# Kernel tuning notes

Hardware: AMD Instinct MI355X
Metric: run time of the kernel (lower is better)

The kernel has to match this reference:

```python
import jax, jax.numpy as jnp
import numpy as np
import math

N_NODES = 50000
N_EDGES = 800000
F_IN = 32
HID = 64


def _layernorm(x, g, b, eps=1e-5):
    mu = x.mean(-1, keepdims=True)
    var = ((x - mu) ** 2).mean(-1, keepdims=True)
    return (x - mu) / jnp.sqrt(var + eps) * g + b


def _tconv(x, src, dst, Wq, bq, Wk, bk, Wv, bv, Ws, heads):
    # PyG TransformerConv (concat=True, root_weight=True, bias=False on skip)
    N = x.shape[0]
    C = Wq.shape[1] // heads
    q = (x @ Wq + bq).reshape(N, heads, C)[dst]  # [E,H,C] gathered at targets
    k = (x @ Wk + bk).reshape(N, heads, C)[src]  # [E,H,C] gathered at sources
    v = (x @ Wv + bv).reshape(N, heads, C)[src]
    scores = (q * k).sum(-1) / math.sqrt(C)      # [E,H]
    m = jax.ops.segment_max(scores, dst, num_segments=N)   # [N,H]
    p = jnp.exp(scores - m[dst])
    denom = jax.ops.segment_sum(p, dst, num_segments=N)
    alpha = p / (denom[dst] + 1e-16)             # segment softmax over in-edges
    agg = jax.ops.segment_sum(v * alpha[..., None], dst, num_segments=N)
    return agg.reshape(N, heads * C) + x @ Ws    # + skip (no bias)


def setup_inputs() -> dict:
    key = jax.random.key(0)
    ks = iter(jax.random.split(key, 64))
    def rn(shape, s=0.1):
        return jax.random.normal(next(ks), shape, jnp.float32) * s
    inp = {
        "x": rn((N_NODES, F_IN), 1.0),
        "edge_index": jax.random.randint(next(ks), (2, N_EDGES), 0, N_NODES, dtype=jnp.int32),
        "ln0_g": jnp.ones((F_IN,), jnp.float32),
        "ln0_b": jnp.zeros((F_IN,), jnp.float32),
    }
    dims = [F_IN, HID, HID]
    for l in range(3):
        d = dims[l]
        inp[f"Wq{l}"] = rn((d, HID)); inp[f"bq{l}"] = rn((HID,), 0.05)
        inp[f"Wk{l}"] = rn((d, HID)); inp[f"bk{l}"] = rn((HID,), 0.05)
        inp[f"Wv{l}"] = rn((d, HID)); inp[f"bv{l}"] = rn((HID,), 0.05)
        inp[f"Ws{l}"] = rn((d, HID))
        inp[f"g{l}"] = jnp.ones((HID,), jnp.float32)
        inp[f"b{l}"] = jnp.zeros((HID,), jnp.float32)
    inp["Wr1"] = rn((HID, HID // 2)); inp["br1"] = jnp.zeros((HID // 2,), jnp.float32)
    inp["Wr2"] = rn((HID // 2, 1));   inp["br2"] = jnp.zeros((1,), jnp.float32)
    inp["Wt1"] = rn((HID, HID // 2)); inp["bt1"] = jnp.zeros((HID // 2,), jnp.float32)
    inp["Wt2"] = rn((HID // 2, 1));   inp["bt2"] = jnp.zeros((1,), jnp.float32)
    return inp


def reference(x, edge_index, ln0_g, ln0_b,
              Wq0, bq0, Wk0, bk0, Wv0, bv0, Ws0, g0, b0,
              Wq1, bq1, Wk1, bk1, Wv1, bv1, Ws1, g1, b1,
              Wq2, bq2, Wk2, bk2, Wv2, bv2, Ws2, g2, b2,
              Wr1, br1, Wr2, br2, Wt1, bt1, Wt2, bt2):
    src, dst = edge_index[0], edge_index[1]
    h = _layernorm(x, ln0_g, ln0_b)
    layers = [
        (Wq0, bq0, Wk0, bk0, Wv0, bv0, Ws0, g0, b0, 4),
        (Wq1, bq1, Wk1, bk1, Wv1, bv1, Ws1, g1, b1, 4),
        (Wq2, bq2, Wk2, bk2, Wv2, bv2, Ws2, g2, b2, 1),
    ]
    for i, (Wq, bq, Wk, bk, Wv, bv, Ws, g, b, heads) in enumerate(layers):
        x_res = h if h.shape[-1] == HID else None
        h = _tconv(h, src, dst, Wq, bq, Wk, bk, Wv, bv, Ws, heads)
        h = _layernorm(h, g, b)
        if x_res is not None and i > 0:
            h = h + 0.1 * x_res
        if i < len(layers) - 1:
            h = jax.nn.relu(h)  # dropout is identity in eval mode
    rtt = jax.nn.relu(h @ Wr1 + br1) @ Wr2 + br2      # [N,1]
    retrans = jax.nn.relu(h @ Wt1 + bt1) @ Wt2 + bt2  # [N,1]
    return jnp.concatenate([rtt, retrans], axis=1)    # [N,2]
```

## Files before the change

kernel.cpp:

```cpp
#include <hip/hip_runtime.h>
#include <hip/hip_bf16.h>
#include <hip/hip_fp16.h>
#include <math.h>

#define N_NODES 50000
#define N_EDGES 800000
#define HID 64
#define NBK 196
#define EPB 1024
#define SB  ((N_EDGES + EPB - 1) / EPB)
#define FLAT (NBK * SB)
#define SCAN_B ((FLAT + 255) / 256)

#define QKVS0_BLKS 3125

#define LN0_BLKS   6250
#define HIST_BLKS  SB
#define WP0_BLKS   32
#define WP12_BLKS  64
#define PREP_BLKS  (LN0_BLKS + HIST_BLKS + WP0_BLKS + 2 * WP12_BLKS)

typedef __attribute__((ext_vector_type(8))) short short8;
typedef __attribute__((ext_vector_type(4))) float float4v;
typedef __attribute__((ext_vector_type(2))) float float2v;

__device__ __forceinline__ unsigned short f32_to_bf16_rne(float f) {
    unsigned int u = __float_as_uint(f);
    unsigned int r = u + 0x7fffu + ((u >> 16) & 1u);
    return (unsigned short)(r >> 16);
}

__device__ __forceinline__ unsigned int f32_to_fp8_byte(float f) {
    return (unsigned int)__builtin_amdgcn_cvt_pk_fp8_f32(f, f, 0, false) & 0xffu;
}
template <bool HI>
__device__ __forceinline__ float2v fp8x2_to_f32(unsigned int w) {
    return __builtin_amdgcn_cvt_pk_f32_fp8((int)w, HI);
}
__device__ __forceinline__ float2 h2_to_f32(unsigned int w) {
    __half2 h = *reinterpret_cast<__half2*>(&w);
    return __half22float2(h);
}

__device__ __forceinline__ void ln0_body(int b, int t,
        const float* __restrict__ x, const float* __restrict__ g,
        const float* __restrict__ bb, float* __restrict__ h0) {
    int lane = t & 63;
    int n = b * 8 + (t >> 6) * 2 + (lane >> 5);
    int c = lane & 31;
    float v = x[n * 32 + c];
    float s = v;
    #pragma unroll
    for (int off = 1; off < 32; off <<= 1) s += __shfl_xor(s, off);
    float mu = s * (1.0f / 32.0f);
    float d = v - mu;
    float vs = d * d;
    #pragma unroll
    for (int off = 1; off < 32; off <<= 1) vs += __shfl_xor(vs, off);
    float var = vs * (1.0f / 32.0f);
    h0[n * 32 + c] = d * rsqrtf(var + 1e-5f) * g[c] + bb[c];
}

__device__ __forceinline__ void wprep_body(int idx, int KS,
        const float* __restrict__ Wq, const float* __restrict__ Wk,
        const float* __restrict__ Wv, const float* __restrict__ Ws,
        unsigned short* __restrict__ Wp) {
    int j = idx & 7;
    int lane = (idx >> 3) & 63;
    int ts = idx >> 9;
    int s = ts % KS;
    int tile = ts / KS;
    int which = tile >> 2;
    int slice = tile & 3;
    int k = s * 32 + ((lane >> 4) * 8) + j;
    int col = slice * 16 + (lane & 15);
    const float* W = (which == 0) ? Wq : (which == 1) ? Wk : (which == 2) ? Wv : Ws;
    Wp[idx] = f32_to_bf16_rne(W[k * 64 + col]);
}

__global__ __launch_bounds__(256) void prep_kernel(
        const float* __restrict__ x, const float* __restrict__ ln0g,
        const float* __restrict__ ln0b, float* __restrict__ h0,
        const int* __restrict__ dst, int* __restrict__ ghist,
        const float* __restrict__ Wq0, const float* __restrict__ Wk0,
        const float* __restrict__ Wv0, const float* __restrict__ Ws0,
        unsigned short* __restrict__ Wp0,
        const float* __restrict__ Wq1, const float* __restrict__ Wk1,
        const float* __restrict__ Wv1, const float* __restrict__ Ws1,
        unsigned short* __restrict__ Wp1,
        const float* __restrict__ Wq2, const float* __restrict__ Wk2,
        const float* __restrict__ Wv2, const float* __restrict__ Ws2,
        unsigned short* __restrict__ Wp2) {
    __shared__ int hist[NBK];
    int b = blockIdx.x;
    int t = threadIdx.x;
    if (b < LN0_BLKS) {
        ln0_body(b, t, x, ln0g, ln0b, h0);
    } else if (b < LN0_BLKS + HIST_BLKS) {
        int i = b - LN0_BLKS;
        for (int k = t; k < NBK; k += 256) hist[k] = 0;
        __syncthreads();
        int e0 = i * EPB;
        #pragma unroll
        for (int r = 0; r < EPB / 256; r++) {
            int e = e0 + r * 256 + t;
            if (e < N_EDGES) atomicAdd(&hist[dst[e] >> 8], 1);
        }
        __syncthreads();
        for (int k = t; k < NBK; k += 256) ghist[k * SB + i] = hist[k];
    } else if (b < LN0_BLKS + HIST_BLKS + WP0_BLKS) {
        int idx = (b - LN0_BLKS - HIST_BLKS) * 256 + t;
        wprep_body(idx, 1, Wq0, Wk0, Wv0, Ws0, Wp0);
    } else if (b < LN0_BLKS + HIST_BLKS + WP0_BLKS + WP12_BLKS) {
        int idx = (b - LN0_BLKS - HIST_BLKS - WP0_BLKS) * 256 + t;
        wprep_body(idx, 2, Wq1, Wk1, Wv1, Ws1, Wp1);
    } else {
        int idx = (b - LN0_BLKS - HIST_BLKS - WP0_BLKS - WP12_BLKS) * 256 + t;
        wprep_body(idx, 2, Wq2, Wk2, Wv2, Ws2, Wp2);
    }
}

__global__ void scan1_kernel(const int* __restrict__ ghist, int* __restrict__ csum) {
    int f = blockIdx.x * 256 + threadIdx.x;
    int v = (f < FLAT) ? ghist[f] : 0;
    #pragma unroll
    for (int off = 1; off < 64; off <<= 1) v += __shfl_xor(v, off);
    __shared__ int ws[4];
    if ((threadIdx.x & 63) == 0) ws[threadIdx.x >> 6] = v;
    __syncthreads();
    if (threadIdx.x == 0) csum[blockIdx.x] = ws[0] + ws[1] + ws[2] + ws[3];
}

__global__ void scan2_kernel(const int* __restrict__ csum, int* __restrict__ coff,
                             int* __restrict__ bbase, int* __restrict__ row_ptr) {
    int lane = threadIdx.x;
    int carry = 0;
    for (int base = 0; base < SCAN_B; base += 64) {
        int i = base + lane;
        int v = (i < SCAN_B) ? csum[i] : 0;
        int incl = v;
        #pragma unroll
        for (int off = 1; off < 64; off <<= 1) {
            int tt = __shfl_up(incl, off);
            if (lane >= off) incl += tt;
        }
        if (i < SCAN_B) coff[i] = carry + incl - v;
        carry += __shfl(incl, 63);
    }
    if (lane == 0) { bbase[NBK] = N_EDGES; row_ptr[N_NODES] = N_EDGES; }
}

__global__ void scan3_kernel(const int* __restrict__ ghist, const int* __restrict__ coff,
                             int* __restrict__ goff, int* __restrict__ bbase) {
    int f = blockIdx.x * 256 + threadIdx.x;
    int lane = threadIdx.x & 63;
    int w = threadIdx.x >> 6;
    int v = (f < FLAT) ? ghist[f] : 0;
    int incl = v;
    #pragma unroll
    for (int off = 1; off < 64; off <<= 1) {
        int tt = __shfl_up(incl, off);
        if (lane >= off) incl += tt;
    }
    __shared__ int ws[4];
    if (lane == 63) ws[w] = incl;
    __syncthreads();
    int woff = 0;
    #pragma unroll
    for (int k = 0; k < 4; k++) if (k < w) woff += ws[k];
    int excl = coff[blockIdx.x] + woff + incl - v;
    if (f < FLAT) {
        goff[f] = excl;
        if (f % SB == 0) bbase[f / SB] = excl;
    }
}

template <int D>
__device__ __forceinline__ void qkvs_body(int bid, int t,
        const float* __restrict__ h,
        const unsigned short* __restrict__ Wp,
        const float* __restrict__ bq, const float* __restrict__ bk,
        const float* __restrict__ bv, float scale,
        float* __restrict__ Qf, float* __restrict__ Sf,
        unsigned int* __restrict__ K8, uint2* __restrict__ Vh) {
    constexpr int KS = D / 32;
    int lane = t & 63;
    int w = t >> 6;
    int n0 = bid * 16;
    int n16 = lane & 15;
    int quad = lane >> 4;
    int col = w * 16 + n16;

    short8 afrag[KS];
    #pragma unroll
    for (int s = 0; s < KS; s++) {
        const float* hp = &h[(n0 + n16) * D + s * 32 + quad * 8];
        float4 a0 = *(const float4*)hp;
        float4 a1 = *(const float4*)(hp + 4);
        short8 af;
        af[0] = (short)f32_to_bf16_rne(a0.x);
        af[1] = (short)f32_to_bf16_rne(a0.y);
        af[2] = (short)f32_to_bf16_rne(a0.z);
        af[3] = (short)f32_to_bf16_rne(a0.w);
        af[4] = (short)f32_to_bf16_rne(a1.x);
        af[5] = (short)f32_to_bf16_rne(a1.y);
        af[6] = (short)f32_to_bf16_rne(a1.z);
        af[7] = (short)f32_to_bf16_rne(a1.w);
        afrag[s] = af;
    }

    float4v accs[4];
    #pragma unroll
    for (int which = 0; which < 4; which++) {
        float4v acc = {0.0f, 0.0f, 0.0f, 0.0f};
        int tile = which * 4 + w;
        #pragma unroll
        for (int s = 0; s < KS; s++) {
            short8 bfrag = *(const short8*)&Wp[((tile * KS + s) * 64 + lane) * 8];
            acc = __builtin_amdgcn_mfma_f32_16x16x32_bf16(afrag[s], bfrag, acc, 0, 0, 0);
        }
        accs[which] = acc;
    }

    float bqc = bq[col], bkc = bk[col], bvc = bv[col];
    int j = n16 & 3;
    int mword = (col >> 2);

    #pragma unroll
    for (int r = 0; r < 4; r++) {
        int node = n0 + quad * 4 + r;
        Qf[node * 64 + col] = (accs[0][r] + bqc) * scale;
        Sf[node * 64 + col] = accs[3][r];
        unsigned int ku = f32_to_fp8_byte(accs[1][r] + bkc) << (8 * j);
        ku |= __shfl_xor(ku, 1); ku |= __shfl_xor(ku, 2);
        unsigned int hb = (unsigned int)__half_as_ushort(__float2half_rn(accs[2][r] + bvc));
        unsigned int vx = (j < 2) ? (hb << (16 * j)) : 0u;
        unsigned int vy = (j >= 2) ? (hb << (16 * (j - 2))) : 0u;
        vx |= __shfl_xor(vx, 1); vx |= __shfl_xor(vx, 2);
        vy |= __shfl_xor(vy, 1); vy |= __shfl_xor(vy, 2);
        if (j == 0) {
            K8[node * 16 + mword] = ku;
            Vh[node * 16 + mword] = make_uint2(vx, vy);
        }
    }
}

template <int D>
__global__ __launch_bounds__(256) void qkvs_mfma_kernel(
        const float* __restrict__ h,
        const unsigned short* __restrict__ Wp,
        const float* __restrict__ bq, const float* __restrict__ bk,
        const float* __restrict__ bv, float scale,
        float* __restrict__ Qf, float* __restrict__ Sf,
        unsigned int* __restrict__ K8, uint2* __restrict__ Vh) {
    qkvs_body<D>(blockIdx.x, threadIdx.x, h, Wp, bq, bk, bv, scale, Qf, Sf, K8, Vh);
}

__global__ __launch_bounds__(256) void scatter_qkvs0_kernel(
        const int* __restrict__ src, const int* __restrict__ dst,
        const int* __restrict__ goff, int2* __restrict__ ebkt,
        const float* __restrict__ h, const unsigned short* __restrict__ Wp,
        const float* __restrict__ bq, const float* __restrict__ bk,
        const float* __restrict__ bv, float scale,
        float* __restrict__ Qf, float* __restrict__ Sf,
        unsigned int* __restrict__ K8, uint2* __restrict__ Vh) {
    __shared__ int hist[NBK];
    int t = threadIdx.x;
    if (blockIdx.x < SB) {
        int i = blockIdx.x;
        for (int k = t; k < NBK; k += 256) hist[k] = 0;
        __syncthreads();
        int e0 = i * EPB;
        #pragma unroll
        for (int r = 0; r < EPB / 256; r++) {
            int e = e0 + r * 256 + t;
            if (e < N_EDGES) {
                int s = src[e], d = dst[e];
                int k = d >> 8;
                int rank = atomicAdd(&hist[k], 1);
                ebkt[goff[k * SB + i] + rank] = make_int2(s, d);
            }
        }
    } else {
        qkvs_body<32>(blockIdx.x - SB, t, h, Wp, bq, bk, bv, scale, Qf, Sf, K8, Vh);
    }
}

__global__ __launch_bounds__(256) void bucket_build_kernel(
        const int2* __restrict__ ebkt, const int* __restrict__ bbase,
        int* __restrict__ row_ptr, int* __restrict__ colb) {
    __shared__ int ldeg[256];
    __shared__ int lcur[256];
    __shared__ int wsum[4];
    int b = blockIdx.x;
    int t = threadIdx.x;
    int cbase = bbase[b];
    int cnt = bbase[b + 1] - cbase;

    ldeg[t] = 0;
    __syncthreads();
    for (int i = t; i < cnt; i += 256) {
        int2 e = ebkt[cbase + i];
        atomicAdd(&ldeg[e.y & 255], 1);
    }
    __syncthreads();

    int lane = t & 63;
    int w = t >> 6;
    int v = ldeg[t];
    int incl = v;
    #pragma unroll
    for (int off = 1; off < 64; off <<= 1) {
        int tt = __shfl_up(incl, off);
        if (lane >= off) incl += tt;
    }
    if (lane == 63) wsum[w] = incl;
    __syncthreads();
    int woff = 0;
    #pragma unroll
    for (int k = 0; k < 4; k++) if (k < w) woff += wsum[k];
    int excl = woff + incl - v;

    int node = b * 256 + t;
    if (node < N_NODES) row_ptr[node] = cbase + excl;
    lcur[t] = excl;
    __syncthreads();

    for (int i = t; i < cnt; i += 256) {
        int2 e = ebkt[cbase + i];
        int r = atomicAdd(&lcur[e.y & 255], 1);
        colb[cbase + r] = e.x;
    }
}

template <int HEADS, bool RES, bool RELU, bool HEAD>
__global__ __launch_bounds__(256) void agg_kernel(
                           const float* __restrict__ Qf,
                           const float* __restrict__ Sf,
                           const unsigned int* __restrict__ K8,
                           const uint2* __restrict__ Vh,
                           const int* __restrict__ row_ptr, const int* __restrict__ colb,
                           const float* __restrict__ g, const float* __restrict__ b,
                           const float* __restrict__ h_in, float* __restrict__ h_out,
                           const float* __restrict__ Wr1, const float* __restrict__ br1,
                           const float* __restrict__ Wr2, const float* __restrict__ br2,
                           const float* __restrict__ Wt1, const float* __restrict__ bt1,
                           const float* __restrict__ Wt2, const float* __restrict__ bt2,
                           float* __restrict__ out) {
    constexpr int C = HID / HEADS;
    int lane = threadIdx.x & 63;
    int m = lane & 15;
    int grp = lane >> 4;
    int n = blockIdx.x * 4 + (threadIdx.x >> 6);

    float4 q4 = *(const float4*)&Qf[n * 64 + 4 * m];

    int beg = row_ptr[n], end = row_ptr[n + 1];

    float ssum = 0.0f;
    float acc0 = 0.0f, acc1 = 0.0f, acc2 = 0.0f, acc3 = 0.0f;

    for (int base = beg; base < end; base += 64) {
        int limit = min(end - base, 64);
        int src_l = (base + lane < end) ? colb[base + lane] : 0;
        for (int sub = 0; sub < limit; sub += 16) {
            int e0 = sub + grp, e1 = sub + 4 + grp, e2 = sub + 8 + grp, e3 = sub + 12 + grp;
            int s0 = __shfl(src_l, e0);
            int s1 = __shfl(src_l, e1);
            int s2 = __shfl(src_l, e2);
            int s3 = __shfl(src_l, e3);
            bool v0ok = e0 < limit, v1ok = e1 < limit, v2ok = e2 < limit, v3ok = e3 < limit;
            unsigned int ka0 = 0, ka1 = 0, ka2 = 0, ka3 = 0;
            uint2 va0 = make_uint2(0, 0), va1 = va0, va2 = va0, va3 = va0;
            if (v0ok) { ka0 = K8[(size_t)s0 * 16 + m]; va0 = Vh[(size_t)s0 * 16 + m]; }
            if (v1ok) { ka1 = K8[(size_t)s1 * 16 + m]; va1 = Vh[(size_t)s1 * 16 + m]; }
            if (v2ok) { ka2 = K8[(size_t)s2 * 16 + m]; va2 = Vh[(size_t)s2 * 16 + m]; }
            if (v3ok) { ka3 = K8[(size_t)s3 * 16 + m]; va3 = Vh[(size_t)s3 * 16 + m]; }

            float2v k0a = fp8x2_to_f32<false>(ka0), k0b = fp8x2_to_f32<true>(ka0);
            float2v k1a = fp8x2_to_f32<false>(ka1), k1b = fp8x2_to_f32<true>(ka1);
            float2v k2a = fp8x2_to_f32<false>(ka2), k2b = fp8x2_to_f32<true>(ka2);
            float2v k3a = fp8x2_to_f32<false>(ka3), k3b = fp8x2_to_f32<true>(ka3);

            float t0 = fmaf(q4.x, k0a.x, fmaf(q4.y, k0a.y,
                       fmaf(q4.z, k0b.x, q4.w * k0b.y)));
            float t1 = fmaf(q4.x, k1a.x, fmaf(q4.y, k1a.y,
                       fmaf(q4.z, k1b.x, q4.w * k1b.y)));
            float t2 = fmaf(q4.x, k2a.x, fmaf(q4.y, k2a.y,
                       fmaf(q4.z, k2b.x, q4.w * k2b.y)));
            float t3 = fmaf(q4.x, k3a.x, fmaf(q4.y, k3a.y,
                       fmaf(q4.z, k3b.x, q4.w * k3b.y)));
            #pragma unroll
            for (int off = 1; off < C / 4; off <<= 1) {
                t0 += __shfl_xor(t0, off);
                t1 += __shfl_xor(t1, off);
                t2 += __shfl_xor(t2, off);
                t3 += __shfl_xor(t3, off);
            }
            float p0 = v0ok ? __expf(t0) : 0.0f;
            float p1 = v1ok ? __expf(t1) : 0.0f;
            float p2 = v2ok ? __expf(t2) : 0.0f;
            float p3 = v3ok ? __expf(t3) : 0.0f;
            ssum += (p0 + p1) + (p2 + p3);

            float2 v0a = h2_to_f32(va0.x), v0b = h2_to_f32(va0.y);
            float2 v1a = h2_to_f32(va1.x), v1b = h2_to_f32(va1.y);
            float2 v2a = h2_to_f32(va2.x), v2b = h2_to_f32(va2.y);
            float2 v3a = h2_to_f32(va3.x), v3b = h2_to_f32(va3.y);

            acc0 = fmaf(p0, v0a.x, fmaf(p1, v1a.x,
                   fmaf(p2, v2a.x, fmaf(p3, v3a.x, acc0))));
            acc1 = fmaf(p0, v0a.y, fmaf(p1, v1a.y,
                   fmaf(p2, v2a.y, fmaf(p3, v3a.y, acc1))));
            acc2 = fmaf(p0, v0b.x, fmaf(p1, v1b.x,
                   fmaf(p2, v2b.x, fmaf(p3, v3b.x, acc2))));
            acc3 = fmaf(p0, v0b.y, fmaf(p1, v1b.y,
                   fmaf(p2, v2b.y, fmaf(p3, v3b.y, acc3))));
        }
    }

    #pragma unroll
    for (int off = 16; off < 64; off <<= 1) {
        ssum += __shfl_xor(ssum, off);
        acc0 += __shfl_xor(acc0, off);
        acc1 += __shfl_xor(acc1, off);
        acc2 += __shfl_xor(acc2, off);
        acc3 += __shfl_xor(acc3, off);
    }

    float inv = 1.0f / (ssum + 1e-16f);
    float4 sv = *(const float4*)&Sf[n * 64 + 4 * m];
    float o0 = fmaf(acc0, inv, sv.x);
    float o1 = fmaf(acc1, inv, sv.y);
    float o2 = fmaf(acc2, inv, sv.z);
    float o3 = fmaf(acc3, inv, sv.w);

    float s = (o0 + o1) + (o2 + o3);
    #pragma unroll
    for (int off = 1; off < 16; off <<= 1) s += __shfl_xor(s, off);
    float mu = s * (1.0f / 64.0f);
    float d0 = o0 - mu, d1 = o1 - mu, d2 = o2 - mu, d3 = o3 - mu;
    float vs = (d0 * d0 + d1 * d1) + (d2 * d2 + d3 * d3);
    #pragma unroll
    for (int off = 1; off < 16; off <<= 1) vs += __shfl_xor(vs, off);
    float rstd = rsqrtf(vs * (1.0f / 64.0f) + 1e-5f);

    float4 gv = *(const float4*)&g[4 * m];
    float4 bv = *(const float4*)&b[4 * m];
    float y0 = d0 * rstd * gv.x + bv.x;
    float y1 = d1 * rstd * gv.y + bv.y;
    float y2 = d2 * rstd * gv.z + bv.z;
    float y3 = d3 * rstd * gv.w + bv.w;
    if (RES) {
        float4 rv = *(const float4*)&h_in[n * 64 + 4 * m];
        y0 = fmaf(0.1f, rv.x, y0);
        y1 = fmaf(0.1f, rv.y, y1);
        y2 = fmaf(0.1f, rv.z, y2);
        y3 = fmaf(0.1f, rv.w, y3);
    }
    if (RELU) {
        y0 = fmaxf(y0, 0.0f); y1 = fmaxf(y1, 0.0f);
        y2 = fmaxf(y2, 0.0f); y3 = fmaxf(y3, 0.0f);
    }

    if (!HEAD) {
        if (grp == 0) {
            float4 yv = make_float4(y0, y1, y2, y3);
            *(float4*)&h_out[n * 64 + 4 * m] = yv;
        }
    } else {
        __shared__ float sh[4][HID];
        int wave = threadIdx.x >> 6;
        if (grp == 0) {
            float4 yv = make_float4(y0, y1, y2, y3);
            *(float4*)&sh[wave][4 * m] = yv;
        }
        __syncthreads();
        int half = lane >> 5;
        int j = lane & 31;
        const float* W1 = half ? Wt1 : Wr1;
        const float* b1 = half ? bt1 : br1;
        const float* W2 = half ? Wt2 : Wr2;
        const float* b2v = half ? bt2 : br2;
        float a = b1[j];
        #pragma unroll 8
        for (int i = 0; i < 64; i++) a = fmaf(sh[wave][i], W1[i * 32 + j], a);
        a = fmaxf(a, 0.0f);
        float r = a * W2[j];
        #pragma unroll
        for (int off = 1; off < 32; off <<= 1) r += __shfl_xor(r, off);
        if (j == 0) out[n * 2 + half] = r + b2v[0];
    }
}

extern "C" void kernel_launch(void* const* d_in, const int* in_sizes, int n_in,
                              void* d_out, int out_size, void* d_ws, size_t ws_size,
                              hipStream_t stream) {
    const float* x    = (const float*)d_in[0];
    const int*   ei   = (const int*)d_in[1];
    const int*   src  = ei;
    const int*   dst  = ei + N_EDGES;
    const float* ln0g = (const float*)d_in[2];
    const float* ln0b = (const float*)d_in[3];

    const float* P[27];
    for (int i = 0; i < 27; i++) P[i] = (const float*)d_in[4 + i];
    const float* Wr1 = (const float*)d_in[31];
    const float* br1 = (const float*)d_in[32];
    const float* Wr2 = (const float*)d_in[33];
    const float* br2 = (const float*)d_in[34];
    const float* Wt1 = (const float*)d_in[35];
    const float* bt1 = (const float*)d_in[36];
    const float* Wt2 = (const float*)d_in[37];
    const float* bt2 = (const float*)d_in[38];

    float* out = (float*)d_out;

    float* hbuf0 = (float*)d_ws;
    float* hbuf1 = hbuf0 + N_NODES * 64;
    float* Qf    = hbuf1 + N_NODES * 64;
    float* Sf    = Qf + N_NODES * 64;
    unsigned int* K8 = (unsigned int*)(Sf + N_NODES * 64);
    uint2* Vh    = (uint2*)(K8 + N_NODES * 16);
    int* row_ptr = (int*)(Vh + N_NODES * 16);
    int* colb    = row_ptr + (N_NODES + 1);
    int* ghist   = colb + N_EDGES;
    int* goff    = ghist + FLAT;
    int* csum    = goff + FLAT;
    int* coff    = csum + SCAN_B;
    int* bbase   = coff + SCAN_B;
    unsigned short* Wp0 = (unsigned short*)(bbase + NBK + 1);
    unsigned short* Wp1 = Wp0 + 16 * 1 * 512;
    unsigned short* Wp2 = Wp1 + 16 * 2 * 512;
    int2* ebkt = (int2*)hbuf1;

    prep_kernel<<<PREP_BLKS, 256, 0, stream>>>(x, ln0g, ln0b, hbuf0,
        dst, ghist,
        P[0],  P[2],  P[4],  P[6],  Wp0,
        P[9],  P[11], P[13], P[15], Wp1,
        P[18], P[20], P[22], P[24], Wp2);
    scan1_kernel<<<SCAN_B, 256, 0, stream>>>(ghist, csum);
    scan2_kernel<<<1, 64, 0, stream>>>(csum, coff, bbase, row_ptr);
    scan3_kernel<<<SCAN_B, 256, 0, stream>>>(ghist, coff, goff, bbase);
    scatter_qkvs0_kernel<<<SB + QKVS0_BLKS, 256, 0, stream>>>(src, dst, goff, ebkt,
        hbuf0, Wp0, P[1], P[3], P[5], 0.25f, Qf, Sf, K8, Vh);
    bucket_build_kernel<<<NBK, 256, 0, stream>>>(ebkt, bbase, row_ptr, colb);

    agg_kernel<4, false, true, false><<<12500, 256, 0, stream>>>(Qf, Sf, K8, Vh,
        row_ptr, colb, P[7], P[8], nullptr, hbuf1,
        Wr1, br1, Wr2, br2, Wt1, bt1, Wt2, bt2, out);

    qkvs_mfma_kernel<64><<<3125, 256, 0, stream>>>(hbuf1, Wp1,
        P[10], P[12], P[14], 0.25f, Qf, Sf, K8, Vh);
    agg_kernel<4, true, true, false><<<12500, 256, 0, stream>>>(Qf, Sf, K8, Vh,
        row_ptr, colb, P[16], P[17], hbuf1, hbuf0,
        Wr1, br1, Wr2, br2, Wt1, bt1, Wt2, bt2, out);

    qkvs_mfma_kernel<64><<<3125, 256, 0, stream>>>(hbuf0, Wp2,
        P[19], P[21], P[23], 0.125f, Qf, Sf, K8, Vh);
    agg_kernel<1, true, false, true><<<12500, 256, 0, stream>>>(Qf, Sf, K8, Vh,
        row_ptr, colb, P[25], P[26], hbuf0, hbuf1,
        Wr1, br1, Wr2, br2, Wt1, bt1, Wt2, bt2, out);
}
```

Before: 330.1 us.

## Split edge scoring into separate per-edge kernel and pack Q/skip as bf16

Moves the attention score computation (q·k dot and exp) out of the node-centric aggregation into a new edge-parallel score kernel that writes per-edge exp scores to a buffer. Q and the skip projection are stored packed as bf16 pairs in one word array instead of two fp32 arrays, and the CSR column array now stores (src,dst) pairs so the score kernel knows each edge's target. The aggregation then only gathers V and the precomputed scores. This trades an extra kernel launch per layer and a large intermediate score buffer write/read for better load balance and fewer shuffles in the aggregation, and lowers Q/skip precision to bf16.

```diff
diff --git a/kernel.cpp b/kernel.cpp
--- a/kernel.cpp
+++ b/kernel.cpp
@@ -13,6 +13,7 @@
 #define SCAN_B ((FLAT + 255) / 256)
 
 #define QKVS0_BLKS 3125
+#define SCORE_BLKS ((N_EDGES * 4) / 256)
 
 #define LN0_BLKS   6250
 #define HIST_BLKS  SB
@@ -181,7 +182,7 @@
         const unsigned short* __restrict__ Wp,
         const float* __restrict__ bq, const float* __restrict__ bk,
         const float* __restrict__ bv, float scale,
-        float* __restrict__ Qf, float* __restrict__ Sf,
+        unsigned int* __restrict__ QS,
         unsigned int* __restrict__ K8, uint2* __restrict__ Vh) {
     constexpr int KS = D / 32;
     int lane = t & 63;
@@ -229,8 +230,9 @@
     #pragma unroll
     for (int r = 0; r < 4; r++) {
         int node = n0 + quad * 4 + r;
-        Qf[node * 64 + col] = (accs[0][r] + bqc) * scale;
-        Sf[node * 64 + col] = accs[3][r];
+        unsigned int qw = f32_to_bf16_rne((accs[0][r] + bqc) * scale);
+        unsigned int sw = f32_to_bf16_rne(accs[3][r]);
+        QS[node * 64 + col] = (sw << 16) | qw;
         unsigned int ku = f32_to_fp8_byte(accs[1][r] + bkc) << (8 * j);
         ku |= __shfl_xor(ku, 1); ku |= __shfl_xor(ku, 2);
         unsigned int hb = (unsigned int)__half_as_ushort(__float2half_rn(accs[2][r] + bvc));
@@ -251,9 +253,9 @@
         const unsigned short* __restrict__ Wp,
         const float* __restrict__ bq, const float* __restrict__ bk,
         const float* __restrict__ bv, float scale,
-        float* __restrict__ Qf, float* __restrict__ Sf,
+        unsigned int* __restrict__ QS,
         unsigned int* __restrict__ K8, uint2* __restrict__ Vh) {
-    qkvs_body<D>(blockIdx.x, threadIdx.x, h, Wp, bq, bk, bv, scale, Qf, Sf, K8, Vh);
+    qkvs_body<D>(blockIdx.x, threadIdx.x, h, Wp, bq, bk, bv, scale, QS, K8, Vh);
 }
 
 __global__ __launch_bounds__(256) void scatter_qkvs0_kernel(
@@ -262,7 +264,7 @@
         const float* __restrict__ h, const unsigned short* __restrict__ Wp,
         const float* __restrict__ bq, const float* __restrict__ bk,
         const float* __restrict__ bv, float scale,
-        float* __restrict__ Qf, float* __restrict__ Sf,
+        unsigned int* __restrict__ QS,
         unsigned int* __restrict__ K8, uint2* __restrict__ Vh) {
     __shared__ int hist[NBK];
     int t = threadIdx.x;
@@ -282,13 +284,13 @@
             }
         }
     } else {
-        qkvs_body<32>(blockIdx.x - SB, t, h, Wp, bq, bk, bv, scale, Qf, Sf, K8, Vh);
+        qkvs_body<32>(blockIdx.x - SB, t, h, Wp, bq, bk, bv, scale, QS, K8, Vh);
     }
 }
 
 __global__ __launch_bounds__(256) void bucket_build_kernel(
         const int2* __restrict__ ebkt, const int* __restrict__ bbase,
-        int* __restrict__ row_ptr, int* __restrict__ colb) {
+        int* __restrict__ row_ptr, int2* __restrict__ colb2) {
     __shared__ int ldeg[256];
     __shared__ int lcur[256];
     __shared__ int wsum[4];
@@ -329,17 +331,69 @@
     for (int i = t; i < cnt; i += 256) {
         int2 e = ebkt[cbase + i];
         int r = atomicAdd(&lcur[e.y & 255], 1);
-        colb[cbase + r] = e.x;
+        colb2[cbase + r] = e;
+    }
+}
+
+template <int HEADS>
+__global__ __launch_bounds__(256) void score_kernel(
+        const unsigned int* __restrict__ QS,
+        const unsigned int* __restrict__ K8,
+        const int2* __restrict__ colb2,
+        float* __restrict__ p) {
+    int gid = blockIdx.x * 256 + threadIdx.x;
+    int e = gid >> 2;
+    int slot = gid & 3;
+    int2 ed = colb2[e];
+    const unsigned int* qp = &QS[(size_t)ed.y * 64 + slot * 16];
+    uint4 qa = *(const uint4*)qp;
+    uint4 qb = *(const uint4*)(qp + 4);
+    uint4 qc = *(const uint4*)(qp + 8);
+    uint4 qd = *(const uint4*)(qp + 12);
+    uint4 kw = *(const uint4*)&K8[(size_t)ed.x * 16 + slot * 4];
+
+    float2v k0 = fp8x2_to_f32<false>(kw.x), k1 = fp8x2_to_f32<true>(kw.x);
+    float2v k2 = fp8x2_to_f32<false>(kw.y), k3 = fp8x2_to_f32<true>(kw.y);
+    float2v k4 = fp8x2_to_f32<false>(kw.z), k5 = fp8x2_to_f32<true>(kw.z);
+    float2v k6 = fp8x2_to_f32<false>(kw.w), k7 = fp8x2_to_f32<true>(kw.w);
+
+    float t;
+    t =      __uint_as_float(qa.x << 16) * k0.x;
+    t = fmaf(__uint_as_float(qa.y << 16), k0.y, t);
+    t = fmaf(__uint_as_float(qa.z << 16), k1.x, t);
+    t = fmaf(__uint_as_float(qa.w << 16), k1.y, t);
+    t = fmaf(__uint_as_float(qb.x << 16), k2.x, t);
+    t = fmaf(__uint_as_float(qb.y << 16), k2.y, t);
+    t = fmaf(__uint_as_float(qb.z << 16), k3.x, t);
+    t = fmaf(__uint_as_float(qb.w << 16), k3.y, t);
+    t = fmaf(__uint_as_float(qc.x << 16), k4.x, t);
+    t = fmaf(__uint_as_float(qc.y << 16), k4.y, t);
+    t = fmaf(__uint_as_float(qc.z << 16), k5.x, t);
+    t = fmaf(__uint_as_float(qc.w << 16), k5.y, t);
+    t = fmaf(__uint_as_float(qd.x << 16), k6.x, t);
+    t = fmaf(__uint_as_float(qd.y << 16), k6.y, t);
+    t = fmaf(__uint_as_float(qd.z << 16), k7.x, t);
+    t = fmaf(__uint_as_float(qd.w << 16), k7.y, t);
+
+    if (HEADS == 1) {
+        t += __shfl_xor(t, 1);
+        t += __shfl_xor(t, 2);
+    }
+    float pv = __expf(t);
+    if (HEADS == 4) {
+        p[(size_t)e * 4 + slot] = pv;
+    } else {
+        if (slot == 0) p[e] = pv;
     }
 }
 
 template <int HEADS, bool RES, bool RELU, bool HEAD>
 __global__ __launch_bounds__(256) void agg_kernel(
-                           const float* __restrict__ Qf,
-                           const float* __restrict__ Sf,
-                           const unsigned int* __restrict__ K8,
+                           const unsigned int* __restrict__ QS,
                            const uint2* __restrict__ Vh,
-                           const int* __restrict__ row_ptr, const int* __restrict__ colb,
+                           const float* __restrict__ p,
+                           const int2* __restrict__ colb2,
+                           const int* __restrict__ row_ptr,
                            const float* __restrict__ g, const float* __restrict__ b,
                            const float* __restrict__ h_in, float* __restrict__ h_out,
                            const float* __restrict__ Wr1, const float* __restrict__ br1,
@@ -347,75 +401,35 @@
                            const float* __restrict__ Wt1, const float* __restrict__ bt1,
                            const float* __restrict__ Wt2, const float* __restrict__ bt2,
                            float* __restrict__ out) {
-    constexpr int C = HID / HEADS;
     int lane = threadIdx.x & 63;
     int m = lane & 15;
     int grp = lane >> 4;
     int n = blockIdx.x * 4 + (threadIdx.x >> 6);
-
-    float4 q4 = *(const float4*)&Qf[n * 64 + 4 * m];
+    int hsel = m >> 2;
 
     int beg = row_ptr[n], end = row_ptr[n + 1];
 
     float ssum = 0.0f;
     float acc0 = 0.0f, acc1 = 0.0f, acc2 = 0.0f, acc3 = 0.0f;
 
-    for (int base = beg; base < end; base += 64) {
-        int limit = min(end - base, 64);
-        int src_l = (base + lane < end) ? colb[base + lane] : 0;
-        for (int sub = 0; sub < limit; sub += 16) {
-            int e0 = sub + grp, e1 = sub + 4 + grp, e2 = sub + 8 + grp, e3 = sub + 12 + grp;
-            int s0 = __shfl(src_l, e0);
-            int s1 = __shfl(src_l, e1);
-            int s2 = __shfl(src_l, e2);
-            int s3 = __shfl(src_l, e3);
-            bool v0ok = e0 < limit, v1ok = e1 < limit, v2ok = e2 < limit, v3ok = e3 < limit;
-            unsigned int ka0 = 0, ka1 = 0, ka2 = 0, ka3 = 0;
-            uint2 va0 = make_uint2(0, 0), va1 = va0, va2 = va0, va3 = va0;
-            if (v0ok) { ka0 = K8[(size_t)s0 * 16 + m]; va0 = Vh[(size_t)s0 * 16 + m]; }
-            if (v1ok) { ka1 = K8[(size_t)s1 * 16 + m]; va1 = Vh[(size_t)s1 * 16 + m]; }
-            if (v2ok) { ka2 = K8[(size_t)s2 * 16 + m]; va2 = Vh[(size_t)s2 * 16 + m]; }
-            if (v3ok) { ka3 = K8[(size_t)s3 * 16 + m]; va3 = Vh[(size_t)s3 * 16 + m]; }
-
-            float2v k0a = fp8x2_to_f32<false>(ka0), k0b = fp8x2_to_f32<true>(ka0);
-            float2v k1a = fp8x2_to_f32<false>(ka1), k1b = fp8x2_to_f32<true>(ka1);
-            float2v k2a = fp8x2_to_f32<false>(ka2), k2b = fp8x2_to_f32<true>(ka2);
-            float2v k3a = fp8x2_to_f32<false>(ka3), k3b = fp8x2_to_f32<true>(ka3);
-
-            float t0 = fmaf(q4.x, k0a.x, fmaf(q4.y, k0a.y,
-                       fmaf(q4.z, k0b.x, q4.w * k0b.y)));
-            float t1 = fmaf(q4.x, k1a.x, fmaf(q4.y, k1a.y,
-                       fmaf(q4.z, k1b.x, q4.w * k1b.y)));
-            float t2 = fmaf(q4.x, k2a.x, fmaf(q4.y, k2a.y,
-                       fmaf(q4.z, k2b.x, q4.w * k2b.y)));
-            float t3 = fmaf(q4.x, k3a.x, fmaf(q4.y, k3a.y,
-                       fmaf(q4.z, k3b.x, q4.w * k3b.y)));
-            #pragma unroll
-            for (int off = 1; off < C / 4; off <<= 1) {
-                t0 += __shfl_xor(t0, off);
-                t1 += __shfl_xor(t1, off);
-                t2 += __shfl_xor(t2, off);
-                t3 += __shfl_xor(t3, off);
+    for (int base = beg; base < end; base += 16) {
+        #pragma unroll
+        for (int c = 0; c < 4; c++) {
+            int idx = base + c * 4 + grp;
+            bool ok = idx < end;
+            int s = 0;
+            float pv = 0.0f;
+            if (ok) {
+                s = colb2[idx].x;
+                pv = (HEADS == 4) ? p[(size_t)idx * 4 + hsel] : p[idx];
             }
-            float p0 = v0ok ? __expf(t0) : 0.0f;
-            float p1 = v1ok ? __expf(t1) : 0.0f;
-            float p2 = v2ok ? __expf(t2) : 0.0f;
-            float p3 = v3ok ? __expf(t3) : 0.0f;
-            ssum += (p0 + p1) + (p2 + p3);
-
-            float2 v0a = h2_to_f32(va0.x), v0b = h2_to_f32(va0.y);
-            float2 v1a = h2_to_f32(va1.x), v1b = h2_to_f32(va1.y);
-            float2 v2a = h2_to_f32(va2.x), v2b = h2_to_f32(va2.y);
-            float2 v3a = h2_to_f32(va3.x), v3b = h2_to_f32(va3.y);
-
-            acc0 = fmaf(p0, v0a.x, fmaf(p1, v1a.x,
-                   fmaf(p2, v2a.x, fmaf(p3, v3a.x, acc0))));
-            acc1 = fmaf(p0, v0a.y, fmaf(p1, v1a.y,
-                   fmaf(p2, v2a.y, fmaf(p3, v3a.y, acc1))));
-            acc2 = fmaf(p0, v0b.x, fmaf(p1, v1b.x,
-                   fmaf(p2, v2b.x, fmaf(p3, v3b.x, acc2))));
-            acc3 = fmaf(p0, v0b.y, fmaf(p1, v1b.y,
-                   fmaf(p2, v2b.y, fmaf(p3, v3b.y, acc3))));
+            uint2 va = Vh[(size_t)s * 16 + m];
+            float2 v0 = h2_to_f32(va.x), v1 = h2_to_f32(va.y);
+            ssum += pv;
+            acc0 = fmaf(pv, v0.x, acc0);
+            acc1 = fmaf(pv, v0.y, acc1);
+            acc2 = fmaf(pv, v1.x, acc2);
+            acc3 = fmaf(pv, v1.y, acc3);
         }
     }
 
@@ -429,11 +443,11 @@
     }
 
     float inv = 1.0f / (ssum + 1e-16f);
-    float4 sv = *(const float4*)&Sf[n * 64 + 4 * m];
-    float o0 = fmaf(acc0, inv, sv.x);
-    float o1 = fmaf(acc1, inv, sv.y);
-    float o2 = fmaf(acc2, inv, sv.z);
-    float o3 = fmaf(acc3, inv, sv.w);
+    uint4 qsw = *(const uint4*)&QS[(size_t)n * 64 + 4 * m];
+    float o0 = fmaf(acc0, inv, __uint_as_float(qsw.x & 0xffff0000u));
+    float o1 = fmaf(acc1, inv, __uint_as_float(qsw.y & 0xffff0000u));
+    float o2 = fmaf(acc2, inv, __uint_as_float(qsw.z & 0xffff0000u));
+    float o3 = fmaf(acc3, inv, __uint_as_float(qsw.w & 0xffff0000u));
 
     float s = (o0 + o1) + (o2 + o3);
     #pragma unroll
@@ -518,13 +532,13 @@
 
     float* hbuf0 = (float*)d_ws;
     float* hbuf1 = hbuf0 + N_NODES * 64;
-    float* Qf    = hbuf1 + N_NODES * 64;
-    float* Sf    = Qf + N_NODES * 64;
-    unsigned int* K8 = (unsigned int*)(Sf + N_NODES * 64);
+    unsigned int* QSb = (unsigned int*)(hbuf1 + N_NODES * 64);
+    unsigned int* K8 = QSb + N_NODES * 64;
     uint2* Vh    = (uint2*)(K8 + N_NODES * 16);
-    int* row_ptr = (int*)(Vh + N_NODES * 16);
-    int* colb    = row_ptr + (N_NODES + 1);
-    int* ghist   = colb + N_EDGES;
+    float* pbuf  = (float*)(Vh + N_NODES * 16);
+    int* row_ptr = (int*)(pbuf + (size_t)N_EDGES * 4);
+    int2* colb2  = (int2*)(row_ptr + (N_NODES + 2));
+    int* ghist   = (int*)(colb2 + N_EDGES);
     int* goff    = ghist + FLAT;
     int* csum    = goff + FLAT;
     int* coff    = csum + SCAN_B;
@@ -543,22 +557,25 @@
     scan2_kernel<<<1, 64, 0, stream>>>(csum, coff, bbase, row_ptr);
     scan3_kernel<<<SCAN_B, 256, 0, stream>>>(ghist, coff, goff, bbase);
     scatter_qkvs0_kernel<<<SB + QKVS0_BLKS, 256, 0, stream>>>(src, dst, goff, ebkt,
-        hbuf0, Wp0, P[1], P[3], P[5], 0.25f, Qf, Sf, K8, Vh);
-    bucket_build_kernel<<<NBK, 256, 0, stream>>>(ebkt, bbase, row_ptr, colb);
-
-    agg_kernel<4, false, true, false><<<12500, 256, 0, stream>>>(Qf, Sf, K8, Vh,
-        row_ptr, colb, P[7], P[8], nullptr, hbuf1,
+        hbuf0, Wp0, P[1], P[3], P[5], 0.25f, QSb, K8, Vh);
+    bucket_build_kernel<<<NBK, 256, 0, stream>>>(ebkt, bbase, row_ptr, colb2);
+
+    score_kernel<4><<<SCORE_BLKS, 256, 0, stream>>>(QSb, K8, colb2, pbuf);
+    agg_kernel<4, false, true, false><<<12500, 256, 0, stream>>>(QSb, Vh, pbuf,
+        colb2, row_ptr, P[7], P[8], nullptr, hbuf1,
         Wr1, br1, Wr2, br2, Wt1, bt1, Wt2, bt2, out);
 
     qkvs_mfma_kernel<64><<<3125, 256, 0, stream>>>(hbuf1, Wp1,
-        P[10], P[12], P[14], 0.25f, Qf, Sf, K8, Vh);
-    agg_kernel<4, true, true, false><<<12500, 256, 0, stream>>>(Qf, Sf, K8, Vh,
-        row_ptr, colb, P[16], P[17], hbuf1, hbuf0,
+        P[10], P[12], P[14], 0.25f, QSb, K8, Vh);
+    score_kernel<4><<<SCORE_BLKS, 256, 0, stream>>>(QSb, K8, colb2, pbuf);
+    agg_kernel<4, true, true, false><<<12500, 256, 0, stream>>>(QSb, Vh, pbuf,
+        colb2, row_ptr, P[16], P[17], hbuf1, hbuf0,
         Wr1, br1, Wr2, br2, Wt1, bt1, Wt2, bt2, out);
 
     qkvs_mfma_kernel<64><<<3125, 256, 0, stream>>>(hbuf0, Wp2,
-        P[19], P[21], P[23], 0.125f, Qf, Sf, K8, Vh);
-    agg_kernel<1, true, false, true><<<12500, 256, 0, stream>>>(Qf, Sf, K8, Vh,
-        row_ptr, colb, P[25], P[26], hbuf0, hbuf1,
+        P[19], P[21], P[23], 0.125f, QSb, K8, Vh);
+    score_kernel<1><<<SCORE_BLKS, 256, 0, stream>>>(QSb, K8, colb2, pbuf);
+    agg_kernel<1, true, false, true><<<12500, 256, 0, stream>>>(QSb, Vh, pbuf,
+        colb2, row_ptr, P[25], P[26], hbuf0, hbuf1,
         Wr1, br1, Wr2, br2, Wt1, bt1, Wt2, bt2, out);
 }
```

After: 382.3 us. 1.16x slower.
